# Performance work log

Hardware: AMD Instinct MI355X
Metric: run time of the kernel (lower is better)

The kernel has to match this reference:

```python
import jax, jax.numpy as jnp
import numpy as np

P = 4   # patch_size
S = 2   # patch_stride


def setup_inputs() -> dict:
    key = jax.random.key(0)
    ks = jax.random.split(key, 7)
    img    = jax.random.uniform(ks[0], (8, 1, 1024, 1024), dtype=jnp.float32)
    w_conv = jax.random.normal(ks[1], (2, 1, 2, 2), dtype=jnp.float32) * 0.5  # Conv2d(1,2,k=2,s=2)
    b_conv = jax.random.normal(ks[2], (2,), dtype=jnp.float32) * 0.1
    W_b    = jax.random.normal(ks[3], (2, 2), dtype=jnp.float32) * 0.5        # Linear(2,2)
    b_b    = jax.random.normal(ks[4], (2,), dtype=jnp.float32) * 0.1
    W_d    = jax.random.normal(ks[5], (2, 1, 2, 2), dtype=jnp.float32) * 0.5  # ConvTranspose2d(2,1,k=2,s=2)
    b_d    = jax.random.normal(ks[6], (1,), dtype=jnp.float32) * 0.1
    return dict(img=img, w_conv=w_conv, b_conv=b_conv, W_b=W_b, b_b=b_b, W_d=W_d, b_d=b_d)


def reference(img, w_conv, b_conv, W_b, b_b, W_d, b_d):
    B, _, H, Wd_ = img.shape
    nj = (H - P) // S + 1
    nk = (Wd_ - P) // S + 1

    # gather indices for patch extraction / overlap-add
    rows = (jnp.arange(nj) * S)[:, None] + jnp.arange(P)[None, :]  # (nj, P)
    cols = (jnp.arange(nk) * S)[:, None] + jnp.arange(P)[None, :]  # (nk, P)
    r = rows[:, None, :, None]  # (nj, 1, P, 1)
    c = cols[None, :, None, :]  # (1, nk, 1, P)

    # extract all overlapping patches: (B, nj, nk, P, P)
    patches = img[:, 0][:, r, c]
    N = B * nj * nk
    p = patches.reshape(N, P, P)

    # Conv2d(1->2, kernel 2, stride 2) + ReLU; non-overlapping 2x2 blocks
    blocks = p.reshape(N, 2, 2, 2, 2)                 # (N, j2, ph, k2, pw)
    conv = jnp.einsum('njpkq,cpq->ncjk', blocks, w_conv[:, 0]) + b_conv[None, :, None, None]
    conv = jax.nn.relu(conv)                          # (N, 2, 2, 2)

    # MaxPool2d(2,2) with indices (row-major within 2x2 window)
    flat = conv.reshape(N, 2, 4)
    idx = jnp.argmax(flat, axis=-1)                   # (N, 2) int
    vals = jnp.max(flat, axis=-1)                     # (N, 2)

    # bottleneck: Linear(2,2) + ReLU
    z = jax.nn.relu(vals @ W_b.T + b_b)               # (N, 2)

    # MaxUnpool2d -> (N, 2, 2, 2)
    unp = (z[..., None] * jax.nn.one_hot(idx, 4, dtype=z.dtype)).reshape(N, 2, 2, 2)

    # ConvTranspose2d(2->1, kernel 2, stride 2) + Sigmoid: out[2i+p, 2j+q]
    dec = jnp.einsum('ncij,cpq->nipjq', unp, W_d[:, 0]).reshape(N, P, P) + b_d[0]
    dec = jax.nn.sigmoid(dec).reshape(B, nj, nk, P, P)

    # overlap-add fold + count normalization
    out = jnp.zeros((B, H, Wd_), dtype=img.dtype).at[:, r, c].add(dec)
    count = jnp.zeros((H, Wd_), dtype=img.dtype).at[r, c].add(1.0)
    return (out / count)[:, None]  # (B, 1, H, W)
```

## Files before the change

### kernel.cpp

```cpp
#include <hip/hip_runtime.h>

#define IMG_H 1024
#define IMG_W 1024
#define TILES 16
#define NPJ 17
#define NPATCH (NPJ * NPJ)
#define PSTR 20

__global__ __launch_bounds__(256) void ae_fused(
    const float* __restrict__ img,
    const float* __restrict__ w_conv,
    const float* __restrict__ b_conv,
    const float* __restrict__ W_b,
    const float* __restrict__ b_b,
    const float* __restrict__ W_d,
    const float* __restrict__ b_d,
    float* __restrict__ out)
{
    __shared__ __align__(16) float dec[NPATCH * PSTR];

    const int t  = threadIdx.x;
    const int n0 = blockIdx.x * TILES;
    const int m0 = blockIdx.y * TILES;
    const int b  = blockIdx.z;

    float wc[2][4], wd[2][4], wb[2][2];
    #pragma unroll
    for (int c = 0; c < 2; ++c) {
        #pragma unroll
        for (int q = 0; q < 4; ++q) {
            wc[c][q] = w_conv[c * 4 + q];
            wd[c][q] = W_d[c * 4 + q];
        }
    }
    wb[0][0] = W_b[0]; wb[0][1] = W_b[1];
    wb[1][0] = W_b[2]; wb[1][1] = W_b[3];
    const float bc0 = b_conv[0], bc1 = b_conv[1];
    const float bb0 = b_b[0],   bb1 = b_b[1];
    const float bd  = b_d[0];

    const float* imgb = img + (size_t)b * IMG_H * IMG_W;

    #pragma unroll
    for (int it = 0; it < 2; ++it) {
        const int lp = t + it * 256;
        if (lp < NPATCH) {
            const int lpj = lp / NPJ;
            const int lpk = lp - lpj * NPJ;
            const int j = m0 - 1 + lpj;
            const int k = n0 - 1 + lpk;
            float* d = &dec[lp * PSTR];
            if (j >= 0 && j <= 510 && k >= 0 && k <= 510) {
                float p[4][4];
                const float* base = imgb + (size_t)(2 * j) * IMG_W + 2 * k;
                #pragma unroll
                for (int r = 0; r < 4; ++r) {
                    const float2 va = *(const float2*)(base + (size_t)r * IMG_W);
                    const float2 vb = *(const float2*)(base + (size_t)r * IMG_W + 2);
                    p[r][0] = va.x; p[r][1] = va.y; p[r][2] = vb.x; p[r][3] = vb.y;
                }
                float v0[4], v1[4];
                #pragma unroll
                for (int jj = 0; jj < 2; ++jj) {
                    #pragma unroll
                    for (int kk = 0; kk < 2; ++kk) {
                        const float p00 = p[2 * jj][2 * kk];
                        const float p01 = p[2 * jj][2 * kk + 1];
                        const float p10 = p[2 * jj + 1][2 * kk];
                        const float p11 = p[2 * jj + 1][2 * kk + 1];
                        const float s0 = p00 * wc[0][0] + p01 * wc[0][1] + p10 * wc[0][2] + p11 * wc[0][3] + bc0;
                        const float s1 = p00 * wc[1][0] + p01 * wc[1][1] + p10 * wc[1][2] + p11 * wc[1][3] + bc1;
                        v0[jj * 2 + kk] = fmaxf(s0, 0.0f);
                        v1[jj * 2 + kk] = fmaxf(s1, 0.0f);
                    }
                }
                int i0 = 0, i1 = 0;
                float mx0 = v0[0], mx1 = v1[0];
                #pragma unroll
                for (int q = 1; q < 4; ++q) {
                    if (v0[q] > mx0) { mx0 = v0[q]; i0 = q; }
                    if (v1[q] > mx1) { mx1 = v1[q]; i1 = q; }
                }
                const float z0 = fmaxf(mx0 * wb[0][0] + mx1 * wb[0][1] + bb0, 0.0f);
                const float z1 = fmaxf(mx0 * wb[1][0] + mx1 * wb[1][1] + bb1, 0.0f);

                const float sc = 1.0f / (1.0f + __expf(-bd));
                const float4 cq = make_float4(sc, sc, sc, sc);
                #pragma unroll
                for (int qd = 0; qd < 4; ++qd) *(float4*)(d + qd * 4) = cq;

                {
                    const float g0 = z0;
                    const float g1 = (i1 == i0) ? z1 : 0.0f;
                    float4 q;
                    q.x = 1.0f / (1.0f + __expf(-(g0 * wd[0][0] + g1 * wd[1][0] + bd)));
                    q.y = 1.0f / (1.0f + __expf(-(g0 * wd[0][1] + g1 * wd[1][1] + bd)));
                    q.z = 1.0f / (1.0f + __expf(-(g0 * wd[0][2] + g1 * wd[1][2] + bd)));
                    q.w = 1.0f / (1.0f + __expf(-(g0 * wd[0][3] + g1 * wd[1][3] + bd)));
                    *(float4*)(d + i0 * 4) = q;
                }
                {
                    const float g0 = (i0 == i1) ? z0 : 0.0f;
                    const float g1 = z1;
                    float4 q;
                    q.x = 1.0f / (1.0f + __expf(-(g0 * wd[0][0] + g1 * wd[1][0] + bd)));
                    q.y = 1.0f / (1.0f + __expf(-(g0 * wd[0][1] + g1 * wd[1][1] + bd)));
                    q.z = 1.0f / (1.0f + __expf(-(g0 * wd[0][2] + g1 * wd[1][2] + bd)));
                    q.w = 1.0f / (1.0f + __expf(-(g0 * wd[0][3] + g1 * wd[1][3] + bd)));
                    *(float4*)(d + i1 * 4) = q;
                }
            } else {
                const float4 zq = make_float4(0.0f, 0.0f, 0.0f, 0.0f);
                #pragma unroll
                for (int qd = 0; qd < 4; ++qd) *(float4*)(d + qd * 4) = zq;
            }
        }
    }
    __syncthreads();

    const int ty = t >> 4, tx = t & 15;
    const int m = m0 + ty, n = n0 + tx;
    float a0 = 0.f, a1 = 0.f, a2 = 0.f, a3 = 0.f;
    #pragma unroll
    for (int a = 0; a < 2; ++a) {
        #pragma unroll
        for (int e = 0; e < 2; ++e) {
            const int lp = (ty + a) * NPJ + (tx + e);
            const int qd = (1 - a) * 2 + (1 - e);
            const float4 q = *(const float4*)(dec + lp * PSTR + qd * 4);
            a0 += q.x; a1 += q.y; a2 += q.z; a3 += q.w;
        }
    }
    const float rcnt = 1.0f / (float)(((m >= 1) + (m <= 510)) * ((n >= 1) + (n <= 510)));
    float* outb = out + (size_t)b * IMG_H * IMG_W;
    *(float2*)(outb + (size_t)(2 * m) * IMG_W + 2 * n)     = make_float2(a0 * rcnt, a1 * rcnt);
    *(float2*)(outb + (size_t)(2 * m + 1) * IMG_W + 2 * n) = make_float2(a2 * rcnt, a3 * rcnt);
}

extern "C" void kernel_launch(void* const* d_in, const int* in_sizes, int n_in,
                              void* d_out, int out_size, void* d_ws, size_t ws_size,
                              hipStream_t stream) {
    const float* img    = (const float*)d_in[0];
    const float* w_conv = (const float*)d_in[1];
    const float* b_conv = (const float*)d_in[2];
    const float* W_b    = (const float*)d_in[3];
    const float* b_b    = (const float*)d_in[4];
    const float* W_d    = (const float*)d_in[5];
    const float* b_d    = (const float*)d_in[6];
    float* out = (float*)d_out;

    dim3 block(256, 1, 1);
    dim3 grid(512 / TILES, 512 / TILES, 8);
    ae_fused<<<grid, block, 0, stream>>>(img, w_conv, b_conv, W_b, b_b, W_d, b_d, out);
}
```

Before: 107.0 us.

## Share conv outputs across overlapping patches via shared-memory stage

Adds a first stage where each thread computes one 2x2-block conv result (both channels) for an 18x18 halo tile and stores it in shared memory. The patch stage then reads four neighbouring conv results instead of loading 16 pixels and recomputing four convolutions per patch. Each conv block is shared by up to four overlapping patches, so this removes redundant global loads and arithmetic. The cost is an extra __syncthreads and more shared memory per block, which may lower occupancy.

```diff
diff --git a/kernel.cpp b/kernel.cpp
--- a/kernel.cpp
+++ b/kernel.cpp
@@ -5,7 +5,13 @@
 #define TILES 16
 #define NPJ 17
 #define NPATCH (NPJ * NPJ)
+#define NCJ 18
+#define NCB (NCJ * NCJ)
 #define PSTR 20
+
+static __device__ __forceinline__ int iclamp(int v, int lo, int hi) {
+    return v < lo ? lo : (v > hi ? hi : v);
+}
 
 __global__ __launch_bounds__(256) void ae_fused(
     const float* __restrict__ img,
@@ -18,6 +24,7 @@
     float* __restrict__ out)
 {
     __shared__ __align__(16) float dec[NPATCH * PSTR];
+    __shared__ __align__(8)  float2 convs[NCB];
 
     const int t  = threadIdx.x;
     const int n0 = blockIdx.x * TILES;
@@ -43,6 +50,25 @@
 
     #pragma unroll
     for (int it = 0; it < 2; ++it) {
+        const int cb = t + it * 256;
+        if (cb < NCB) {
+            const int cj = cb / NCJ;
+            const int ck = cb - cj * NCJ;
+            const int J = iclamp(m0 - 1 + cj, 0, 511);
+            const int K = iclamp(n0 - 1 + ck, 0, 511);
+            const float* base = imgb + (size_t)(2 * J) * IMG_W + 2 * K;
+            const float2 r0 = *(const float2*)(base);
+            const float2 r1 = *(const float2*)(base + IMG_W);
+            const float s0 = r0.x * wc[0][0] + r0.y * wc[0][1] + r1.x * wc[0][2] + r1.y * wc[0][3] + bc0;
+            const float s1 = r0.x * wc[1][0] + r0.y * wc[1][1] + r1.x * wc[1][2] + r1.y * wc[1][3] + bc1;
+            convs[cb] = make_float2(fmaxf(s0, 0.0f), fmaxf(s1, 0.0f));
+        }
+    }
+    __syncthreads();
+
+    const float sc = 1.0f / (1.0f + __expf(-bd));
+    #pragma unroll
+    for (int it = 0; it < 2; ++it) {
         const int lp = t + it * 256;
         if (lp < NPATCH) {
             const int lpj = lp / NPJ;
@@ -51,29 +77,14 @@
             const int k = n0 - 1 + lpk;
             float* d = &dec[lp * PSTR];
             if (j >= 0 && j <= 510 && k >= 0 && k <= 510) {
-                float p[4][4];
-                const float* base = imgb + (size_t)(2 * j) * IMG_W + 2 * k;
-                #pragma unroll
-                for (int r = 0; r < 4; ++r) {
-                    const float2 va = *(const float2*)(base + (size_t)r * IMG_W);
-                    const float2 vb = *(const float2*)(base + (size_t)r * IMG_W + 2);
-                    p[r][0] = va.x; p[r][1] = va.y; p[r][2] = vb.x; p[r][3] = vb.y;
-                }
-                float v0[4], v1[4];
-                #pragma unroll
-                for (int jj = 0; jj < 2; ++jj) {
-                    #pragma unroll
-                    for (int kk = 0; kk < 2; ++kk) {
-                        const float p00 = p[2 * jj][2 * kk];
-                        const float p01 = p[2 * jj][2 * kk + 1];
-                        const float p10 = p[2 * jj + 1][2 * kk];
-                        const float p11 = p[2 * jj + 1][2 * kk + 1];
-                        const float s0 = p00 * wc[0][0] + p01 * wc[0][1] + p10 * wc[0][2] + p11 * wc[0][3] + bc0;
-                        const float s1 = p00 * wc[1][0] + p01 * wc[1][1] + p10 * wc[1][2] + p11 * wc[1][3] + bc1;
-                        v0[jj * 2 + kk] = fmaxf(s0, 0.0f);
-                        v1[jj * 2 + kk] = fmaxf(s1, 0.0f);
-                    }
-                }
+                const int cbase = lpj * NCJ + lpk;
+                const float2 c00 = convs[cbase];
+                const float2 c01 = convs[cbase + 1];
+                const float2 c10 = convs[cbase + NCJ];
+                const float2 c11 = convs[cbase + NCJ + 1];
+                const float v0[4] = { c00.x, c01.x, c10.x, c11.x };
+                const float v1[4] = { c00.y, c01.y, c10.y, c11.y };
+
                 int i0 = 0, i1 = 0;
                 float mx0 = v0[0], mx1 = v1[0];
                 #pragma unroll
@@ -84,7 +95,6 @@
                 const float z0 = fmaxf(mx0 * wb[0][0] + mx1 * wb[0][1] + bb0, 0.0f);
                 const float z1 = fmaxf(mx0 * wb[1][0] + mx1 * wb[1][1] + bb1, 0.0f);
 
-                const float sc = 1.0f / (1.0f + __expf(-bd));
                 const float4 cq = make_float4(sc, sc, sc, sc);
                 #pragma unroll
                 for (int qd = 0; qd < 4; ++qd) *(float4*)(d + qd * 4) = cq;
```

After: 109.5 us. 1.02x slower.

## Store decoded patches in shared memory as packed fp16 and use exp2 sigmoid

Applied to the files above, without the earlier changes.

The decoded patch buffer in shared memory switches from fp32 to packed half2, halving LDS footprint and traffic, and the overlap-add accumulation now runs in packed fp16. Sigmoid is rewritten to use exp2f with weights prescaled by -log2(e), and the patch stores become branch-selected half2 writes instead of overwriting stores. Image loads move into the conv loop. The fp16 storage and accumulation with round-toward-zero conversion lowers accuracy, which may exceed tolerance.

```diff
diff --git a/kernel.cpp b/kernel.cpp
--- a/kernel.cpp
+++ b/kernel.cpp
@@ -5,7 +5,16 @@
 #define TILES 16
 #define NPJ 17
 #define NPATCH (NPJ * NPJ)
-#define PSTR 20
+#define PSTRH 20
+
+typedef __attribute__((ext_vector_type(2))) __fp16 h2;
+
+static __device__ __forceinline__ float h2_as_f(h2 v) {
+    union { h2 h; float f; } u; u.h = v; return u.f;
+}
+static __device__ __forceinline__ h2 f_as_h2(float f) {
+    union { float f; h2 h; } u; u.f = f; return u.h;
+}
 
 __global__ __launch_bounds__(256) void ae_fused(
     const float* __restrict__ img,
@@ -17,27 +26,31 @@
     const float* __restrict__ b_d,
     float* __restrict__ out)
 {
-    __shared__ __align__(16) float dec[NPATCH * PSTR];
+    __shared__ __align__(16) __fp16 dec[NPATCH * PSTRH];
 
     const int t  = threadIdx.x;
     const int n0 = blockIdx.x * TILES;
     const int m0 = blockIdx.y * TILES;
     const int b  = blockIdx.z;
 
-    float wc[2][4], wd[2][4], wb[2][2];
+    const float LOG2E = 1.4426950408889634f;
+    float wc[2][4], nwd[2][4], wb[2][2];
     #pragma unroll
     for (int c = 0; c < 2; ++c) {
         #pragma unroll
         for (int q = 0; q < 4; ++q) {
-            wc[c][q] = w_conv[c * 4 + q];
-            wd[c][q] = W_d[c * 4 + q];
+            wc[c][q]  = w_conv[c * 4 + q];
+            nwd[c][q] = -W_d[c * 4 + q] * LOG2E;
         }
     }
     wb[0][0] = W_b[0]; wb[0][1] = W_b[1];
     wb[1][0] = W_b[2]; wb[1][1] = W_b[3];
     const float bc0 = b_conv[0], bc1 = b_conv[1];
     const float bb0 = b_b[0],   bb1 = b_b[1];
-    const float bd  = b_d[0];
+    const float nbd = -b_d[0] * LOG2E;
+    const float scf = 1.0f / (1.0f + exp2f(nbd));
+    const h2 ch = { (__fp16)scf, (__fp16)scf };
+    const h2 zh = { (__fp16)0.0f, (__fp16)0.0f };
 
     const float* imgb = img + (size_t)b * IMG_H * IMG_W;
 
@@ -49,27 +62,18 @@
             const int lpk = lp - lpj * NPJ;
             const int j = m0 - 1 + lpj;
             const int k = n0 - 1 + lpk;
-            float* d = &dec[lp * PSTR];
+            __fp16* d = &dec[lp * PSTRH];
             if (j >= 0 && j <= 510 && k >= 0 && k <= 510) {
-                float p[4][4];
                 const float* base = imgb + (size_t)(2 * j) * IMG_W + 2 * k;
-                #pragma unroll
-                for (int r = 0; r < 4; ++r) {
-                    const float2 va = *(const float2*)(base + (size_t)r * IMG_W);
-                    const float2 vb = *(const float2*)(base + (size_t)r * IMG_W + 2);
-                    p[r][0] = va.x; p[r][1] = va.y; p[r][2] = vb.x; p[r][3] = vb.y;
-                }
                 float v0[4], v1[4];
                 #pragma unroll
                 for (int jj = 0; jj < 2; ++jj) {
                     #pragma unroll
                     for (int kk = 0; kk < 2; ++kk) {
-                        const float p00 = p[2 * jj][2 * kk];
-                        const float p01 = p[2 * jj][2 * kk + 1];
-                        const float p10 = p[2 * jj + 1][2 * kk];
-                        const float p11 = p[2 * jj + 1][2 * kk + 1];
-                        const float s0 = p00 * wc[0][0] + p01 * wc[0][1] + p10 * wc[0][2] + p11 * wc[0][3] + bc0;
-                        const float s1 = p00 * wc[1][0] + p01 * wc[1][1] + p10 * wc[1][2] + p11 * wc[1][3] + bc1;
+                        const float2 ra = *(const float2*)(base + (size_t)(2 * jj) * IMG_W + 2 * kk);
+                        const float2 rb = *(const float2*)(base + (size_t)(2 * jj + 1) * IMG_W + 2 * kk);
+                        const float s0 = ra.x * wc[0][0] + ra.y * wc[0][1] + rb.x * wc[0][2] + rb.y * wc[0][3] + bc0;
+                        const float s1 = ra.x * wc[1][0] + ra.y * wc[1][1] + rb.x * wc[1][2] + rb.y * wc[1][3] + bc1;
                         v0[jj * 2 + kk] = fmaxf(s0, 0.0f);
                         v1[jj * 2 + kk] = fmaxf(s1, 0.0f);
                     }
@@ -84,35 +88,29 @@
                 const float z0 = fmaxf(mx0 * wb[0][0] + mx1 * wb[0][1] + bb0, 0.0f);
                 const float z1 = fmaxf(mx0 * wb[1][0] + mx1 * wb[1][1] + bb1, 0.0f);
 
-                const float sc = 1.0f / (1.0f + __expf(-bd));
-                const float4 cq = make_float4(sc, sc, sc, sc);
+                const float ag1 = (i1 == i0) ? z1 : 0.0f;
+                const float bg0 = (i0 == i1) ? z0 : 0.0f;
+                float av[4], bv[4];
                 #pragma unroll
-                for (int qd = 0; qd < 4; ++qd) *(float4*)(d + qd * 4) = cq;
-
-                {
-                    const float g0 = z0;
-                    const float g1 = (i1 == i0) ? z1 : 0.0f;
-                    float4 q;
-                    q.x = 1.0f / (1.0f + __expf(-(g0 * wd[0][0] + g1 * wd[1][0] + bd)));
-                    q.y = 1.0f / (1.0f + __expf(-(g0 * wd[0][1] + g1 * wd[1][1] + bd)));
-                    q.z = 1.0f / (1.0f + __expf(-(g0 * wd[0][2] + g1 * wd[1][2] + bd)));
-                    q.w = 1.0f / (1.0f + __expf(-(g0 * wd[0][3] + g1 * wd[1][3] + bd)));
-                    *(float4*)(d + i0 * 4) = q;
+                for (int q = 0; q < 4; ++q) {
+                    av[q] = 1.0f / (1.0f + exp2f(z0 * nwd[0][q] + ag1 * nwd[1][q] + nbd));
+                    bv[q] = 1.0f / (1.0f + exp2f(bg0 * nwd[0][q] + z1 * nwd[1][q] + nbd));
                 }
-                {
-                    const float g0 = (i0 == i1) ? z0 : 0.0f;
-                    const float g1 = z1;
-                    float4 q;
-                    q.x = 1.0f / (1.0f + __expf(-(g0 * wd[0][0] + g1 * wd[1][0] + bd)));
-                    q.y = 1.0f / (1.0f + __expf(-(g0 * wd[0][1] + g1 * wd[1][1] + bd)));
-                    q.z = 1.0f / (1.0f + __expf(-(g0 * wd[0][2] + g1 * wd[1][2] + bd)));
-                    q.w = 1.0f / (1.0f + __expf(-(g0 * wd[0][3] + g1 * wd[1][3] + bd)));
-                    *(float4*)(d + i1 * 4) = q;
+                const h2 a01 = __builtin_amdgcn_cvt_pkrtz(av[0], av[1]);
+                const h2 a23 = __builtin_amdgcn_cvt_pkrtz(av[2], av[3]);
+                const h2 b01 = __builtin_amdgcn_cvt_pkrtz(bv[0], bv[1]);
+                const h2 b23 = __builtin_amdgcn_cvt_pkrtz(bv[2], bv[3]);
+                #pragma unroll
+                for (int qd = 0; qd < 4; ++qd) {
+                    const h2 q01 = (qd == i1) ? b01 : ((qd == i0) ? a01 : ch);
+                    const h2 q23 = (qd == i1) ? b23 : ((qd == i0) ? a23 : ch);
+                    float2 w; w.x = h2_as_f(q01); w.y = h2_as_f(q23);
+                    *(float2*)(d + 4 * qd) = w;
                 }
             } else {
-                const float4 zq = make_float4(0.0f, 0.0f, 0.0f, 0.0f);
+                float2 zw; zw.x = h2_as_f(zh); zw.y = h2_as_f(zh);
                 #pragma unroll
-                for (int qd = 0; qd < 4; ++qd) *(float4*)(d + qd * 4) = zq;
+                for (int qd = 0; qd < 4; ++qd) *(float2*)(d + 4 * qd) = zw;
             }
         }
     }
@@ -120,21 +118,24 @@
 
     const int ty = t >> 4, tx = t & 15;
     const int m = m0 + ty, n = n0 + tx;
-    float a0 = 0.f, a1 = 0.f, a2 = 0.f, a3 = 0.f;
+    h2 s01 = zh, s23 = zh;
     #pragma unroll
     for (int a = 0; a < 2; ++a) {
         #pragma unroll
         for (int e = 0; e < 2; ++e) {
             const int lp = (ty + a) * NPJ + (tx + e);
             const int qd = (1 - a) * 2 + (1 - e);
-            const float4 q = *(const float4*)(dec + lp * PSTR + qd * 4);
-            a0 += q.x; a1 += q.y; a2 += q.z; a3 += q.w;
+            const float2 w = *(const float2*)(dec + lp * PSTRH + 4 * qd);
+            s01 += f_as_h2(w.x);
+            s23 += f_as_h2(w.y);
         }
     }
     const float rcnt = 1.0f / (float)(((m >= 1) + (m <= 510)) * ((n >= 1) + (n <= 510)));
     float* outb = out + (size_t)b * IMG_H * IMG_W;
-    *(float2*)(outb + (size_t)(2 * m) * IMG_W + 2 * n)     = make_float2(a0 * rcnt, a1 * rcnt);
-    *(float2*)(outb + (size_t)(2 * m + 1) * IMG_W + 2 * n) = make_float2(a2 * rcnt, a3 * rcnt);
+    *(float2*)(outb + (size_t)(2 * m) * IMG_W + 2 * n) =
+        make_float2((float)s01.x * rcnt, (float)s01.y * rcnt);
+    *(float2*)(outb + (size_t)(2 * m + 1) * IMG_W + 2 * n) =
+        make_float2((float)s23.x * rcnt, (float)s23.y * rcnt);
 }
 
 extern "C" void kernel_launch(void* const* d_in, const int* in_sizes, int n_in,
```

Measured after the change: 112.1 us. 1.05x slower.
